# Optimization experiments

Measured on AMD Instinct MI355X. Metric: run time of the kernel, lower is better.

Reference implementation:

```python
import jax, jax.numpy as jnp
import numpy as np

B, T, C, E = 4, 2048, 1024, 8  # batch, seq, n_embd, num_experts


def setup_inputs() -> dict:
    key = jax.random.key(0)
    k_x, k_wr, k_we = jax.random.split(key, 3)
    x = jax.random.normal(k_x, (B, T, C), dtype=jnp.float32)
    # router: Linear(C, E); scale chosen so softmax gates spread around the 0.5 threshold
    Wr = jax.random.normal(k_wr, (E, C), dtype=jnp.float32) * 0.05
    br = jnp.zeros((E,), dtype=jnp.float32)
    # experts: E x Linear(C, C), y = x @ W^T + b
    We = jax.random.normal(k_we, (E, C, C), dtype=jnp.float32) * (1.0 / np.sqrt(C))
    be = jnp.zeros((E, C), dtype=jnp.float32)
    return {"x": x, "Wr": Wr, "br": br, "We": We, "be": be}


def reference(x, Wr, br, We, be):
    # router logits + softmax gates: [B, T, E]
    logits = jnp.einsum('btc,ec->bte', x, Wr) + br
    gates = jax.nn.softmax(logits, axis=-1)
    # hard selection: token goes through expert e iff gate_e > 0.5 (at most one
    # expert per token since gates sum to 1); output is NOT scaled by the gate.
    mask = (gates > 0.5).astype(x.dtype)  # [B, T, E]
    # all-expert outputs (torch Linear: y = x @ W^T + b): [B, T, E, C]
    h = jnp.einsum('btc,edc->bted', x, We) + be
    # masked combine -> [B, T, C]; unrouted tokens stay zero like torch.zeros_like
    return jnp.einsum('bted,bte->btd', h, mask)
```

## Files before the change

### kernel.cpp

```cpp
#include <hip/hip_runtime.h>
#include <hip/hip_bf16.h>
#include <stdint.h>

#define NB 4
#define NT 2048
#define NC 1024
#define NE 8
#define NTOK (NB * NT)
#define MAXT (NTOK / 128 + NE - 1)
#define CSTRIDE 32

typedef __attribute__((ext_vector_type(4))) float floatx4;
typedef __attribute__((ext_vector_type(8))) __bf16 bf16x8;
typedef __attribute__((ext_vector_type(4))) __bf16 bf16x4;
typedef unsigned short ushort_t;

#define AS1 __attribute__((address_space(1)))
#define AS3 __attribute__((address_space(3)))

__device__ __forceinline__ ushort_t f2bf(float f) {
    uint32_t u = __builtin_bit_cast(uint32_t, f);
    u += 0x7FFFu + ((u >> 16) & 1u);
    return (ushort_t)(u >> 16);
}

__global__ void zero_counts_k(int* __restrict__ counts) {
    if (threadIdx.x < NE) counts[threadIdx.x * CSTRIDE] = 0;
}

__global__ __launch_bounds__(256, 4) void router_conv_k(
    const float* __restrict__ x, const float* __restrict__ Wr,
    const float* __restrict__ br, float* __restrict__ out,
    int* __restrict__ counts, int* __restrict__ buckets,
    ushort_t* __restrict__ xbf,
    const float* __restrict__ We, ushort_t* __restrict__ webf)
{
    const int bid = blockIdx.x;

    if (bid & 1) {
        const int cb = bid >> 1;
        const size_t cbase = ((size_t)(cb * 256 + threadIdx.x)) * 8;
        {
            float4 a = *(const float4*)(We + cbase);
            float4 b = *(const float4*)(We + cbase + 4);
            union { bf16x8 v; ushort_t s[8]; } p;
            p.s[0] = f2bf(a.x); p.s[1] = f2bf(a.y); p.s[2] = f2bf(a.z); p.s[3] = f2bf(a.w);
            p.s[4] = f2bf(b.x); p.s[5] = f2bf(b.y); p.s[6] = f2bf(b.z); p.s[7] = f2bf(b.w);
            *(bf16x8*)(webf + cbase) = p.v;
        }
        {
            float4 a = *(const float4*)(We + cbase + 4194304);
            float4 b = *(const float4*)(We + cbase + 4194304 + 4);
            union { bf16x8 v; ushort_t s[8]; } p;
            p.s[0] = f2bf(a.x); p.s[1] = f2bf(a.y); p.s[2] = f2bf(a.z); p.s[3] = f2bf(a.w);
            p.s[4] = f2bf(b.x); p.s[5] = f2bf(b.y); p.s[6] = f2bf(b.z); p.s[7] = f2bf(b.w);
            *(bf16x8*)(webf + cbase + 4194304) = p.v;
        }
        return;
    }

    const int wave = threadIdx.x >> 6;
    const int lane = threadIdx.x & 63;
    const int tok  = (bid >> 1) * 4 + wave;

    const float4* xr = (const float4*)(x + (size_t)tok * NC);
    float4 xv[4];
#pragma unroll
    for (int j = 0; j < 4; ++j) xv[j] = xr[lane + 64 * j];

    float acc[NE];
#pragma unroll
    for (int e = 0; e < NE; ++e) {
        const float4* wr = (const float4*)(Wr + e * NC);
        float a = 0.f;
#pragma unroll
        for (int j = 0; j < 4; ++j) {
            float4 w = wr[lane + 64 * j];
            a += xv[j].x * w.x; a += xv[j].y * w.y;
            a += xv[j].z * w.z; a += xv[j].w * w.w;
        }
        acc[e] = a;
    }
#pragma unroll
    for (int off = 32; off >= 1; off >>= 1)
#pragma unroll
        for (int e = 0; e < NE; ++e) acc[e] += __shfl_xor(acc[e], off);

#pragma unroll
    for (int e = 0; e < NE; ++e) acc[e] += br[e];

    float lmax = acc[0]; int emax = 0;
#pragma unroll
    for (int e = 1; e < NE; ++e) if (acc[e] > lmax) { lmax = acc[e]; emax = e; }
    float S = 0.f;
#pragma unroll
    for (int e = 0; e < NE; ++e) S += expf(acc[e] - lmax);

    const bool routed = (S < 2.0f);
    if (routed) {
        union { bf16x4 v; ushort_t s[4]; } p;
#pragma unroll
        for (int j = 0; j < 4; ++j) {
            p.s[0] = f2bf(xv[j].x); p.s[1] = f2bf(xv[j].y);
            p.s[2] = f2bf(xv[j].z); p.s[3] = f2bf(xv[j].w);
            *(bf16x4*)(xbf + (size_t)tok * NC + (lane + 64 * j) * 4) = p.v;
        }
        if (lane == 0) {
            int pos = atomicAdd(&counts[emax * CSTRIDE], 1);
            buckets[emax * NTOK + pos] = tok;
        }
    } else {
        float4 z = make_float4(0.f, 0.f, 0.f, 0.f);
        float4* orow = (float4*)(out + (size_t)tok * NC);
#pragma unroll
        for (int j = 0; j < 4; ++j) orow[lane + 64 * j] = z;
    }
}

__global__ __launch_bounds__(256, 4) void router_k(
    const float* __restrict__ x, const float* __restrict__ Wr,
    const float* __restrict__ br, float* __restrict__ out,
    int* __restrict__ counts, int* __restrict__ buckets)
{
    const int wave = threadIdx.x >> 6;
    const int lane = threadIdx.x & 63;
    const int tok  = blockIdx.x * 4 + wave;

    const float4* xr = (const float4*)(x + (size_t)tok * NC);
    float4 xv[4];
#pragma unroll
    for (int j = 0; j < 4; ++j) xv[j] = xr[lane + 64 * j];

    float acc[NE];
#pragma unroll
    for (int e = 0; e < NE; ++e) {
        const float4* wr = (const float4*)(Wr + e * NC);
        float a = 0.f;
#pragma unroll
        for (int j = 0; j < 4; ++j) {
            float4 w = wr[lane + 64 * j];
            a += xv[j].x * w.x; a += xv[j].y * w.y;
            a += xv[j].z * w.z; a += xv[j].w * w.w;
        }
        acc[e] = a;
    }
#pragma unroll
    for (int off = 32; off >= 1; off >>= 1)
#pragma unroll
        for (int e = 0; e < NE; ++e) acc[e] += __shfl_xor(acc[e], off);
#pragma unroll
    for (int e = 0; e < NE; ++e) acc[e] += br[e];

    float lmax = acc[0]; int emax = 0;
#pragma unroll
    for (int e = 1; e < NE; ++e) if (acc[e] > lmax) { lmax = acc[e]; emax = e; }
    float S = 0.f;
#pragma unroll
    for (int e = 0; e < NE; ++e) S += expf(acc[e] - lmax);

    if (S < 2.0f) {
        if (lane == 0) {
            int pos = atomicAdd(&counts[emax * CSTRIDE], 1);
            buckets[emax * NTOK + pos] = tok;
        }
    } else {
        float4 z = make_float4(0.f, 0.f, 0.f, 0.f);
        float4* orow = (float4*)(out + (size_t)tok * NC);
#pragma unroll
        for (int j = 0; j < 4; ++j) orow[lane + 64 * j] = z;
    }
}

__device__ __forceinline__ void gload_lds16(const void* g, void* l) {
    __builtin_amdgcn_global_load_lds((const AS1 unsigned int*)g,
                                     (AS3 unsigned int*)l, 16, 0, 0);
}

__global__ __launch_bounds__(256) void moe_gemm_bf16_k(
    const ushort_t* __restrict__ xbf, const ushort_t* __restrict__ webf,
    const float* __restrict__ be, float* __restrict__ out,
    const int* __restrict__ counts, const int* __restrict__ buckets)
{
    int cw[NE];
#pragma unroll
    for (int i = 0; i < NE; ++i) cw[i] = counts[i * CSTRIDE];
    const int t = blockIdx.x;
    int base = 0, e = -1, m0 = 0;
#pragma unroll
    for (int i = 0; i < NE; ++i) {
        const int te = (cw[i] + 127) >> 7;
        if (e < 0 && t < base + te) { e = i; m0 = (t - base) << 7; }
        base += te;
    }
    if (e < 0) return;
    const int cnt = cw[e];
    const int n0  = blockIdx.y * 128;

    __shared__ ushort_t As[128 * 64];
    __shared__ ushort_t Bs[128 * 64];

    const int tid   = threadIdx.x;
    const int wave  = tid >> 6, lane = tid & 63;
    const int chunk = tid & 7;
    const int rbase = tid >> 3;

    const ushort_t* asrc[4];
    const ushort_t* bsrc[4];
#pragma unroll
    for (int i = 0; i < 4; ++i) {
        const int row = i * 32 + rbase;
        const int sc  = chunk ^ (row & 7);
        int mi = m0 + row; if (mi >= cnt) mi = cnt - 1;
        const int tok = buckets[e * NTOK + mi];
        asrc[i] = xbf + (size_t)tok * NC + sc * 8;
        bsrc[i] = webf + ((size_t)(e * 1024 + n0 + row)) * NC + sc * 8;
    }

    const int wm = (wave >> 1) * 64, wn = (wave & 1) * 64;
    const int fr = lane & 15, hi = lane >> 4;

    floatx4 acc[4][4];
#pragma unroll
    for (int m = 0; m < 4; ++m)
#pragma unroll
        for (int n = 0; n < 4; ++n) acc[m][n] = (floatx4)(0.0f);

    for (int k0 = 0; k0 < NC; k0 += 64) {
#pragma unroll
        for (int i = 0; i < 4; ++i)
            gload_lds16(asrc[i] + k0, &As[(i * 256 + tid) * 8]);
#pragma unroll
        for (int i = 0; i < 4; ++i)
            gload_lds16(bsrc[i] + k0, &Bs[(i * 256 + tid) * 8]);
        __syncthreads();
#pragma unroll
        for (int ks = 0; ks < 2; ++ks) {
            bf16x8 af[4], bfv[4];
#pragma unroll
            for (int m = 0; m < 4; ++m) {
                const int row = wm + m * 16 + fr;
                const int cg  = (ks * 4 + hi) ^ (row & 7);
                af[m] = *(const bf16x8*)((const char*)As + row * 128 + cg * 16);
            }
#pragma unroll
            for (int n = 0; n < 4; ++n) {
                const int row = wn + n * 16 + fr;
                const int cg  = (ks * 4 + hi) ^ (row & 7);
                bfv[n] = *(const bf16x8*)((const char*)Bs + row * 128 + cg * 16);
            }
#pragma unroll
            for (int m = 0; m < 4; ++m)
#pragma unroll
                for (int n = 0; n < 4; ++n)
                    acc[m][n] = __builtin_amdgcn_mfma_f32_16x16x32_bf16(
                        af[m], bfv[n], acc[m][n], 0, 0, 0);
        }
        __syncthreads();
    }

    const int r4 = (lane >> 4) * 4;
    float bev[4];
#pragma unroll
    for (int n = 0; n < 4; ++n) bev[n] = be[e * NC + n0 + wn + n * 16 + fr];
#pragma unroll
    for (int m = 0; m < 4; ++m) {
#pragma unroll
        for (int j = 0; j < 4; ++j) {
            const int trow = m0 + wm + m * 16 + r4 + j;
            if (trow < cnt) {
                const int tok = buckets[e * NTOK + trow];
                float* orow = out + (size_t)tok * NC + n0 + wn + fr;
#pragma unroll
                for (int n = 0; n < 4; ++n) orow[n * 16] = acc[m][n][j] + bev[n];
            }
        }
    }
}

#define BM 64
#define BN 64
#define BK 32
#define LPAD 40
__global__ __launch_bounds__(256) void moe_gemm_k(
    const float* __restrict__ x, const float* __restrict__ We,
    const float* __restrict__ be, float* __restrict__ out,
    const int* __restrict__ counts, const int* __restrict__ buckets)
{
    const int e   = blockIdx.z;
    const int cnt = counts[e * CSTRIDE];
    const int m0  = blockIdx.x * BM;
    if (m0 >= cnt) return;
    const int n0  = blockIdx.y * BN;

    __shared__ ushort_t As[BM * LPAD];
    __shared__ ushort_t Bs[BM * LPAD];

    const int tid  = threadIdx.x;
    const int srow = tid >> 2;
    const int scg  = (tid & 3) * 8;

    const int mrow = m0 + srow;
    const int tokA = (mrow < cnt) ? buckets[e * NTOK + mrow] : -1;
    const float* xrow = x + (size_t)(tokA < 0 ? 0 : tokA) * NC;
    const float* wrow = We + ((size_t)e * NC + (n0 + srow)) * NC;

    const int wave = tid >> 6, lane = tid & 63;
    const int wm = (wave >> 1) * 32, wn = (wave & 1) * 32;
    const int fr = lane & 15;
    const int fk = (lane >> 4) * 8;

    floatx4 acc[2][2];
#pragma unroll
    for (int m = 0; m < 2; ++m)
#pragma unroll
        for (int n = 0; n < 2; ++n) acc[m][n] = (floatx4)(0.0f);

    for (int k0 = 0; k0 < NC; k0 += BK) {
        float4 a0 = make_float4(0.f,0.f,0.f,0.f), a1 = a0;
        if (tokA >= 0) {
            a0 = *(const float4*)(xrow + k0 + scg);
            a1 = *(const float4*)(xrow + k0 + scg + 4);
        }
        float4 b0 = *(const float4*)(wrow + k0 + scg);
        float4 b1 = *(const float4*)(wrow + k0 + scg + 4);

        __syncthreads();
        union { bf16x8 v; ushort_t s[8]; } pa, pb;
        pa.s[0] = f2bf(a0.x); pa.s[1] = f2bf(a0.y); pa.s[2] = f2bf(a0.z); pa.s[3] = f2bf(a0.w);
        pa.s[4] = f2bf(a1.x); pa.s[5] = f2bf(a1.y); pa.s[6] = f2bf(a1.z); pa.s[7] = f2bf(a1.w);
        pb.s[0] = f2bf(b0.x); pb.s[1] = f2bf(b0.y); pb.s[2] = f2bf(b0.z); pb.s[3] = f2bf(b0.w);
        pb.s[4] = f2bf(b1.x); pb.s[5] = f2bf(b1.y); pb.s[6] = f2bf(b1.z); pb.s[7] = f2bf(b1.w);
        *(bf16x8*)&As[srow * LPAD + scg] = pa.v;
        *(bf16x8*)&Bs[srow * LPAD + scg] = pb.v;
        __syncthreads();

        bf16x8 af[2], bfr[2];
#pragma unroll
        for (int m = 0; m < 2; ++m)
            af[m] = *(const bf16x8*)&As[(wm + m * 16 + fr) * LPAD + fk];
#pragma unroll
        for (int n = 0; n < 2; ++n)
            bfr[n] = *(const bf16x8*)&Bs[(wn + n * 16 + fr) * LPAD + fk];
#pragma unroll
        for (int m = 0; m < 2; ++m)
#pragma unroll
            for (int n = 0; n < 2; ++n)
                acc[m][n] = __builtin_amdgcn_mfma_f32_16x16x32_bf16(af[m], bfr[n], acc[m][n], 0, 0, 0);
    }

    const int r4 = (lane >> 4) * 4;
#pragma unroll
    for (int m = 0; m < 2; ++m) {
        const int trowb = m0 + wm + m * 16 + r4;
#pragma unroll
        for (int j = 0; j < 4; ++j) {
            const int trow = trowb + j;
            if (trow < cnt) {
                const int tok = buckets[e * NTOK + trow];
#pragma unroll
                for (int n = 0; n < 2; ++n) {
                    const int d = n0 + wn + n * 16 + fr;
                    out[(size_t)tok * NC + d] = acc[m][n][j] + be[e * NC + d];
                }
            }
        }
    }
}

extern "C" void kernel_launch(void* const* d_in, const int* in_sizes, int n_in,
                              void* d_out, int out_size, void* d_ws, size_t ws_size,
                              hipStream_t stream)
{
    const float* x  = (const float*)d_in[0];
    const float* Wr = (const float*)d_in[1];
    const float* br = (const float*)d_in[2];
    const float* We = (const float*)d_in[3];
    const float* be = (const float*)d_in[4];
    float* out = (float*)d_out;

    int* counts  = (int*)d_ws;
    int* buckets = (int*)((char*)d_ws + 1024);
    const size_t XBF_OFF = 263168;
    const size_t WBF_OFF = 17040384;
    const size_t WS_NEED = 33817600;
    const bool fast = (ws_size >= WS_NEED);

    hipLaunchKernelGGL(zero_counts_k, dim3(1), dim3(64), 0, stream, counts);
    if (fast) {
        ushort_t* xbf  = (ushort_t*)((char*)d_ws + XBF_OFF);
        ushort_t* webf = (ushort_t*)((char*)d_ws + WBF_OFF);
        hipLaunchKernelGGL(router_conv_k, dim3(NTOK / 2), dim3(256), 0, stream,
                           x, Wr, br, out, counts, buckets, xbf, We, webf);
        hipLaunchKernelGGL(moe_gemm_bf16_k, dim3(MAXT, NC / 128, 1), dim3(256),
                           0, stream, xbf, webf, be, out, counts, buckets);
    } else {
        hipLaunchKernelGGL(router_k, dim3(NTOK / 4), dim3(256), 0, stream,
                           x, Wr, br, out, counts, buckets);
        hipLaunchKernelGGL(moe_gemm_k, dim3(NTOK / BM, NC / BN, NE), dim3(256),
                           0, stream, x, We, be, out, counts, buckets);
    }
}
```

Before: 63.10 us.

## Route four tokens per wave and separate router blocks from weight-conversion blocks

Each router wave now handles four tokens instead of one, reusing each loaded router-weight vector across the four tokens so Wr traffic and load instructions drop. Router blocks (512) are now contiguous and come before the 2048 weight-conversion blocks, instead of alternating with them. The bf16 copy of x is now written for every token, not only routed ones. This adds extra writes and register pressure, and the router work is spread over fewer blocks.

```diff
diff --git a/kernel.cpp b/kernel.cpp
--- a/kernel.cpp
+++ b/kernel.cpp
@@ -9,6 +9,7 @@
 #define NTOK (NB * NT)
 #define MAXT (NTOK / 128 + NE - 1)
 #define CSTRIDE 32
+#define RBLK 512
 
 typedef __attribute__((ext_vector_type(4))) float floatx4;
 typedef __attribute__((ext_vector_type(8))) __bf16 bf16x8;
@@ -37,8 +38,8 @@
 {
     const int bid = blockIdx.x;
 
-    if (bid & 1) {
-        const int cb = bid >> 1;
+    if (bid >= RBLK) {
+        const int cb = bid - RBLK;
         const size_t cbase = ((size_t)(cb * 256 + threadIdx.x)) * 8;
         {
             float4 a = *(const float4*)(We + cbase);
@@ -61,59 +62,83 @@
 
     const int wave = threadIdx.x >> 6;
     const int lane = threadIdx.x & 63;
-    const int tok  = (bid >> 1) * 4 + wave;
-
-    const float4* xr = (const float4*)(x + (size_t)tok * NC);
-    float4 xv[4];
-#pragma unroll
-    for (int j = 0; j < 4; ++j) xv[j] = xr[lane + 64 * j];
-
-    float acc[NE];
-#pragma unroll
-    for (int e = 0; e < NE; ++e) {
-        const float4* wr = (const float4*)(Wr + e * NC);
-        float a = 0.f;
-#pragma unroll
-        for (int j = 0; j < 4; ++j) {
-            float4 w = wr[lane + 64 * j];
-            a += xv[j].x * w.x; a += xv[j].y * w.y;
-            a += xv[j].z * w.z; a += xv[j].w * w.w;
-        }
-        acc[e] = a;
-    }
+    const int tb   = (bid * 4 + wave) * 4;
+
+    float acc[4][NE];
+#pragma unroll
+    for (int t = 0; t < 4; ++t)
+#pragma unroll
+        for (int e = 0; e < NE; ++e) acc[t][e] = 0.f;
+
+#pragma unroll
+    for (int h = 0; h < 2; ++h) {
+        float4 xv[4][2];
+#pragma unroll
+        for (int t = 0; t < 4; ++t) {
+            const float4* xr = (const float4*)(x + (size_t)(tb + t) * NC);
+#pragma unroll
+            for (int jh = 0; jh < 2; ++jh)
+                xv[t][jh] = xr[lane + 64 * (h * 2 + jh)];
+        }
+#pragma unroll
+        for (int t = 0; t < 4; ++t) {
+            union { bf16x4 v; ushort_t s[4]; } p;
+#pragma unroll
+            for (int jh = 0; jh < 2; ++jh) {
+                const int j = h * 2 + jh;
+                p.s[0] = f2bf(xv[t][jh].x); p.s[1] = f2bf(xv[t][jh].y);
+                p.s[2] = f2bf(xv[t][jh].z); p.s[3] = f2bf(xv[t][jh].w);
+                *(bf16x4*)(xbf + (size_t)(tb + t) * NC + (lane + 64 * j) * 4) = p.v;
+            }
+        }
+#pragma unroll
+        for (int e = 0; e < NE; ++e) {
+            const float4* wr = (const float4*)(Wr + e * NC);
+            float4 w0 = wr[lane + 64 * (h * 2 + 0)];
+            float4 w1 = wr[lane + 64 * (h * 2 + 1)];
+#pragma unroll
+            for (int t = 0; t < 4; ++t) {
+                float a = acc[t][e];
+                a += xv[t][0].x * w0.x; a += xv[t][0].y * w0.y;
+                a += xv[t][0].z * w0.z; a += xv[t][0].w * w0.w;
+                a += xv[t][1].x * w1.x; a += xv[t][1].y * w1.y;
+                a += xv[t][1].z * w1.z; a += xv[t][1].w * w1.w;
+                acc[t][e] = a;
+            }
+        }
+    }
+
 #pragma unroll
     for (int off = 32; off >= 1; off >>= 1)
 #pragma unroll
-        for (int e = 0; e < NE; ++e) acc[e] += __shfl_xor(acc[e], off);
-
-#pragma unroll
-    for (int e = 0; e < NE; ++e) acc[e] += br[e];
-
-    float lmax = acc[0]; int emax = 0;
-#pragma unroll
-    for (int e = 1; e < NE; ++e) if (acc[e] > lmax) { lmax = acc[e]; emax = e; }
-    float S = 0.f;
-#pragma unroll
-    for (int e = 0; e < NE; ++e) S += expf(acc[e] - lmax);
-
-    const bool routed = (S < 2.0f);
-    if (routed) {
-        union { bf16x4 v; ushort_t s[4]; } p;
-#pragma unroll
-        for (int j = 0; j < 4; ++j) {
-            p.s[0] = f2bf(xv[j].x); p.s[1] = f2bf(xv[j].y);
-            p.s[2] = f2bf(xv[j].z); p.s[3] = f2bf(xv[j].w);
-            *(bf16x4*)(xbf + (size_t)tok * NC + (lane + 64 * j) * 4) = p.v;
-        }
-        if (lane == 0) {
-            int pos = atomicAdd(&counts[emax * CSTRIDE], 1);
-            buckets[emax * NTOK + pos] = tok;
-        }
-    } else {
-        float4 z = make_float4(0.f, 0.f, 0.f, 0.f);
-        float4* orow = (float4*)(out + (size_t)tok * NC);
-#pragma unroll
-        for (int j = 0; j < 4; ++j) orow[lane + 64 * j] = z;
+        for (int t = 0; t < 4; ++t)
+#pragma unroll
+            for (int e = 0; e < NE; ++e) acc[t][e] += __shfl_xor(acc[t][e], off);
+
+#pragma unroll
+    for (int t = 0; t < 4; ++t) {
+#pragma unroll
+        for (int e = 0; e < NE; ++e) acc[t][e] += br[e];
+
+        float lmax = acc[t][0]; int emax = 0;
+#pragma unroll
+        for (int e = 1; e < NE; ++e) if (acc[t][e] > lmax) { lmax = acc[t][e]; emax = e; }
+        float S = 0.f;
+#pragma unroll
+        for (int e = 0; e < NE; ++e) S += expf(acc[t][e] - lmax);
+
+        const bool routed = (S < 2.0f);
+        if (routed) {
+            if (lane == 0) {
+                int pos = atomicAdd(&counts[emax * CSTRIDE], 1);
+                buckets[emax * NTOK + pos] = tb + t;
+            }
+        } else {
+            float4 z = make_float4(0.f, 0.f, 0.f, 0.f);
+            float4* orow = (float4*)(out + (size_t)(tb + t) * NC);
+#pragma unroll
+            for (int j = 0; j < 4; ++j) orow[lane + 64 * j] = z;
+        }
     }
 }
 
@@ -389,7 +414,7 @@
     if (fast) {
         ushort_t* xbf  = (ushort_t*)((char*)d_ws + XBF_OFF);
         ushort_t* webf = (ushort_t*)((char*)d_ws + WBF_OFF);
-        hipLaunchKernelGGL(router_conv_k, dim3(NTOK / 2), dim3(256), 0, stream,
+        hipLaunchKernelGGL(router_conv_k, dim3(RBLK + 2048), dim3(256), 0, stream,
                            x, Wr, br, out, counts, buckets, xbf, We, webf);
         hipLaunchKernelGGL(moe_gemm_bf16_k, dim3(MAXT, NC / 128, 1), dim3(256),
                            0, stream, xbf, webf, be, out, counts, buckets);
```

Measured after the change: 62.59 us. About the same (-0.8%).
